# Kernel tuning notes

Hardware: AMD Instinct MI355X
Metric: run time of the kernel (lower is better)

Reference implementation:

```python
import jax, jax.numpy as jnp
import numpy as np

S, B, I, H, L = 256, 64, 512, 512, 2
EPS = 1e-5


def _layer_norm(x, g, b):
    m = jnp.mean(x, axis=-1, keepdims=True)
    v = jnp.var(x, axis=-1, keepdims=True)
    return (x - m) * jax.lax.rsqrt(v + EPS) * g + b


def setup_inputs() -> dict:
    key = jax.random.key(0)
    ks = jax.random.split(key, 8)
    gain = float(np.sqrt(1.0 / H))
    inputs = jax.random.normal(ks[0], (S, B, I), dtype=jnp.float32)
    h0 = jnp.zeros((L, B, H), dtype=jnp.float32)
    c0 = jnp.zeros((L, B, H), dtype=jnp.float32)
    # stacked weights (input_size == hidden_size so wx is uniform across layers)
    wx = jax.random.uniform(ks[1], (L, I, 4 * H), minval=-gain, maxval=gain, dtype=jnp.float32)
    wh = jax.random.uniform(ks[2], (L, H, 4 * H), minval=-gain, maxval=gain, dtype=jnp.float32)
    bias = jax.random.uniform(ks[3], (L, 4 * H), minval=-gain, maxval=gain, dtype=jnp.float32)
    # LayerNorm affine params: norm[2l] applied to x@wx, norm[2l+1] applied to h@wh
    ln_gx = jnp.ones((L, 4 * H), dtype=jnp.float32)
    ln_bx = jnp.zeros((L, 4 * H), dtype=jnp.float32)
    ln_gh = jnp.ones((L, 4 * H), dtype=jnp.float32)
    ln_bh = jnp.zeros((L, 4 * H), dtype=jnp.float32)
    return {"inputs": inputs, "h0": h0, "c0": c0, "wx": wx, "wh": wh,
            "bias": bias, "ln_gx": ln_gx, "ln_bx": ln_bx, "ln_gh": ln_gh, "ln_bh": ln_bh}


def reference(inputs, h0, c0, wx, wh, bias, ln_gx, ln_bx, ln_gh, ln_bh):
    x = inputs  # [S, B, I]
    hs, cs = [], []
    for l in range(L):
        # input-to-gate projection + its LayerNorm is time-independent: precompute
        xw = jnp.einsum('sbi,io->sbo', x, wx[l])            # [S, B, 4H]
        xn = _layer_norm(xw, ln_gx[l], ln_bx[l]) + bias[l]  # [S, B, 4H]
        whl, gh, bh = wh[l], ln_gh[l], ln_bh[l]

        def step(carry, xt):
            h, c = carry
            gate = xt + _layer_norm(h @ whl, gh, bh)        # [B, 4H]
            i, f, o, u = jnp.split(gate, 4, axis=-1)
            c = jax.nn.sigmoid(f) * c + jax.nn.sigmoid(i) * jnp.tanh(u)
            h = jax.nn.sigmoid(o) * jnp.tanh(c)
            return (h, c), h

        (hN, cN), ys = jax.lax.scan(step, (h0[l], c0[l]), xn)
        hs.append(hN)
        cs.append(cN)
        x = ys  # [S, B, H]
    h_n = jnp.stack(hs, axis=0)  # [L, B, H]
    c_n = jnp.stack(cs, axis=0)
    return x, h_n, c_n
```

## Files before the change

### kernel.cpp

```cpp
#include <hip/hip_runtime.h>

typedef unsigned short u16;
typedef _Float16 f16;
typedef __attribute__((ext_vector_type(8))) _Float16 f16x8;
typedef __attribute__((ext_vector_type(8))) unsigned short u16x8;
typedef __attribute__((ext_vector_type(4))) float f32x4;
typedef __attribute__((ext_vector_type(4))) unsigned u32x4;

#define NWG 32

__device__ __forceinline__ unsigned split2(float v) {
  f16 h = (f16)v;
  f16 l2 = (f16)((v - (float)h) * 2048.0f);
  return (unsigned)__builtin_bit_cast(u16, h) | ((unsigned)__builtin_bit_cast(u16, l2) << 16);
}

__global__ void k_zero(unsigned long long* __restrict__ ist, unsigned* __restrict__ flg) {
  int i = blockIdx.x * blockDim.x + threadIdx.x;
  if (i < 256) ist[i] = 0ull;
  if (i < 8192) flg[i] = 0u;
}

__global__ void k_wsplit(const float* __restrict__ wx, u16* __restrict__ th, u16* __restrict__ tl) {
  __shared__ float tile[32][33];
  int l = blockIdx.z;
  int n0 = blockIdx.x * 32, k0 = blockIdx.y * 32;
  int tx = threadIdx.x, ty = threadIdx.y;
  const float* src = wx + (size_t)l * 512 * 2048;
#pragma unroll
  for (int i = 0; i < 4; ++i)
    tile[ty + i * 8][tx] = src[(size_t)(k0 + ty + i * 8) * 2048 + n0 + tx];
  __syncthreads();
  u16* dh = th + (size_t)l * 2048 * 512;
  u16* dl = tl + (size_t)l * 2048 * 512;
#pragma unroll
  for (int i = 0; i < 4; ++i) {
    unsigned s = split2(tile[tx][ty + i * 8]);
    dh[(size_t)(n0 + ty + i * 8) * 512 + k0 + tx] = (u16)s;
    dl[(size_t)(n0 + ty + i * 8) * 512 + k0 + tx] = (u16)(s >> 16);
  }
}

__global__ void k_wlo(const float* __restrict__ wh, u16* __restrict__ wlo) {
  int idx = blockIdx.x * blockDim.x + threadIdx.x;
  int l = idx >> 17;
  int r = idx & 131071;
  int lane = r & 63;
  int fg = r >> 6;
  int kc = fg & 15, q = (fg >> 4) & 3, g = fg >> 6;
  int gcol = g * 16 + (lane & 15) + q * 512;
  int kb = kc * 32 + ((lane >> 4) << 3);
  const float* W = wh + (size_t)l * 512 * 2048;
  u16x8 o;
#pragma unroll
  for (int j = 0; j < 8; ++j)
    o[j] = (u16)(split2(W[(size_t)(kb + j) * 2048 + gcol]) >> 16);
  *(u16x8*)(wlo + (size_t)idx * 8) = o;
}

__global__ void __launch_bounds__(256, 1) k_gemm3(const float* __restrict__ A,
                                                  const u16* __restrict__ Bh, const u16* __restrict__ Bl,
                                                  float* __restrict__ C, int N, int K) {
  __shared__ u16 sA[2][128 * 64];
  __shared__ u16 sB[2][128 * 64];
  const int tid = threadIdx.x, l = tid & 63, w = tid >> 6;
  const int bx = blockIdx.x, by = blockIdx.y;
  const int wr = (w >> 1) * 64, wc = (w & 1) * 64;
  f32x4 acc0[4][4] = {}, acc1[4][4] = {};
  for (int k0 = 0; k0 < K; k0 += 64) {
#pragma unroll
    for (int s = 0; s < 4; ++s) {
      int cn = s * 256 + tid;
      int row = cn >> 3;
      int f0 = (cn & 7) * 8;
      int kb = f0 * 2;
      int sw = row * 128 + (kb ^ ((row & 7) << 4));
      const float* ap = A + ((size_t)(by * 128 + row) * K + k0 + f0);
      float4 a0 = *(const float4*)ap, a1 = *(const float4*)(ap + 4);
      float av[8] = {a0.x, a0.y, a0.z, a0.w, a1.x, a1.y, a1.z, a1.w};
      u16x8 ah_, al_;
#pragma unroll
      for (int j = 0; j < 8; ++j) {
        unsigned sp = split2(av[j]);
        ah_[j] = (u16)sp;
        al_[j] = (u16)(sp >> 16);
      }
      *(u16x8*)((char*)sA[0] + sw) = ah_;
      *(u16x8*)((char*)sA[1] + sw) = al_;
      size_t gb = (((size_t)(bx * 128 + row) * K + k0) << 1) + kb;
      *(u16x8*)((char*)sB[0] + sw) = *(const u16x8*)((const char*)Bh + gb);
      *(u16x8*)((char*)sB[1] + sw) = *(const u16x8*)((const char*)Bl + gb);
    }
    __syncthreads();
#pragma unroll
    for (int kc = 0; kc < 2; ++kc) {
      int kb = kc * 64 + (l >> 4) * 16;
      f16x8 ah[4], al[4], bh[4], bl[4];
#pragma unroll
      for (int mt = 0; mt < 4; ++mt) {
        int row = wr + mt * 16 + (l & 15);
        int off = row * 128 + (kb ^ ((row & 7) << 4));
        ah[mt] = *(const f16x8*)((const char*)sA[0] + off);
        al[mt] = *(const f16x8*)((const char*)sA[1] + off);
      }
#pragma unroll
      for (int nt = 0; nt < 4; ++nt) {
        int col = wc + nt * 16 + (l & 15);
        int off = col * 128 + (kb ^ ((col & 7) << 4));
        bh[nt] = *(const f16x8*)((const char*)sB[0] + off);
        bl[nt] = *(const f16x8*)((const char*)sB[1] + off);
      }
#pragma unroll
      for (int mt = 0; mt < 4; ++mt)
#pragma unroll
        for (int nt = 0; nt < 4; ++nt) {
          acc0[mt][nt] = __builtin_amdgcn_mfma_f32_16x16x32_f16(ah[mt], bh[nt], acc0[mt][nt], 0, 0, 0);
          acc1[mt][nt] = __builtin_amdgcn_mfma_f32_16x16x32_f16(ah[mt], bl[nt], acc1[mt][nt], 0, 0, 0);
          acc1[mt][nt] = __builtin_amdgcn_mfma_f32_16x16x32_f16(al[mt], bh[nt], acc1[mt][nt], 0, 0, 0);
        }
    }
    __syncthreads();
  }
#pragma unroll
  for (int mt = 0; mt < 4; ++mt)
#pragma unroll
    for (int nt = 0; nt < 4; ++nt)
#pragma unroll
      for (int j = 0; j < 4; ++j) {
        int row = by * 128 + wr + mt * 16 + ((l >> 4) << 2) + j;
        int col = bx * 128 + wc + nt * 16 + (l & 15);
        C[(size_t)row * N + col] = acc0[mt][nt][j] + acc1[mt][nt][j] * (1.0f / 2048.0f);
      }
}

__global__ void __launch_bounds__(256) k_ln2(float* __restrict__ X, const float* __restrict__ g,
                                             const float* __restrict__ b, const float* __restrict__ bias) {
  const int row = blockIdx.x, tid = threadIdx.x;
  float* rp = X + (size_t)row * 2048 + tid * 8;
  float4 v0 = *(const float4*)rp, v1 = *(const float4*)(rp + 4);
  float x[8] = {v0.x, v0.y, v0.z, v0.w, v1.x, v1.y, v1.z, v1.w};
  float s1 = 0.f, s2 = 0.f;
#pragma unroll
  for (int j = 0; j < 8; ++j) { s1 += x[j]; s2 += x[j] * x[j]; }
#pragma unroll
  for (int m = 1; m <= 32; m <<= 1) { s1 += __shfl_xor(s1, m, 64); s2 += __shfl_xor(s2, m, 64); }
  __shared__ float a1[4], a2[4];
  if ((tid & 63) == 0) { a1[tid >> 6] = s1; a2[tid >> 6] = s2; }
  __syncthreads();
  s1 = a1[0] + a1[1] + a1[2] + a1[3];
  s2 = a2[0] + a2[1] + a2[2] + a2[3];
  float mu = s1 * (1.f / 2048.f);
  float var = s2 * (1.f / 2048.f) - mu * mu;
  float rstd = 1.0f / sqrtf(var + 1e-5f);
#pragma unroll
  for (int j = 0; j < 8; ++j) {
    int c = tid * 8 + j;
    x[j] = (x[j] - mu) * rstd * g[c] + b[c] + bias[c];
  }
  *(float4*)rp = {x[0], x[1], x[2], x[3]};
  *(float4*)(rp + 4) = {x[4], x[5], x[6], x[7]};
}

__global__ void __launch_bounds__(256, 1) k_scan4(
    const float* __restrict__ wh, const u16* __restrict__ wlo,
    const float* __restrict__ gh, const float* __restrict__ bh,
    const float* __restrict__ xn, const float* __restrict__ h0l, const float* __restrict__ c0l,
    unsigned* __restrict__ hpubp, float* __restrict__ cspill,
    unsigned long long* __restrict__ istats, unsigned* __restrict__ flags,
    float* __restrict__ ys, float* __restrict__ hn, float* __restrict__ cn,
    int t0, int first) {
  __shared__ u16 pk[32768];
  __shared__ float musd[128];
  const int tid = threadIdx.x;
  const int l = tid & 63, w = tid >> 6;
  const int g = blockIdx.x;
  const int lq = l >> 4, ll = l & 15;
  const int hcol = g * 16 + ll;

  for (int c = tid; c < 4096; c += 256) {
    int lane = c & 63, kc = (c >> 6) & 15, q = c >> 10;
    int gcol = g * 16 + (lane & 15) + q * 512;
    int kb = kc * 32 + ((lane >> 4) << 3);
    u16x8 t8;
#pragma unroll
    for (int j = 0; j < 8; ++j)
      t8[j] = __builtin_bit_cast(u16, (f16)wh[(size_t)(kb + j) * 2048 + gcol]);
    *(u16x8*)(pk + (size_t)c * 8) = t8;
  }
  const u16* wloG = wlo + (size_t)g * 32768;
  float gam[4], bet[4];
#pragma unroll
  for (int q = 0; q < 4; ++q) { int gc = hcol + q * 512; gam[q] = gh[gc]; bet[q] = bh[gc]; }
  float cr[4];
#pragma unroll
  for (int j = 0; j < 4; ++j) {
    int r = w * 16 + lq * 4 + j;
    cr[j] = first ? c0l[r * 512 + hcol] : cspill[r * 512 + hcol];
  }
  if (first) {
    for (int u = tid; u < 1024; u += 256) {
      int row = 2 * g + (u >> 9), col = u & 511;
      __hip_atomic_store(&hpubp[row * 512 + col], split2(h0l[row * 512 + col]),
                         __ATOMIC_RELAXED, __HIP_MEMORY_SCOPE_AGENT);
    }
  }
  unsigned bid = 0;
#define BAR_ARRIVE()                                                                         \
  do {                                                                                       \
    bid++;                                                                                   \
    asm volatile("s_waitcnt vmcnt(0)" ::: "memory");                                         \
    __syncthreads();                                                                         \
    if (tid == 0)                                                                            \
      __hip_atomic_store(&flags[g * 32], bid, __ATOMIC_RELAXED, __HIP_MEMORY_SCOPE_AGENT);   \
  } while (0)
#define BAR_WAIT()                                                                           \
  do {                                                                                       \
    if (tid < NWG)                                                                           \
      while (__hip_atomic_load(&flags[tid * 32], __ATOMIC_RELAXED,                           \
                               __HIP_MEMORY_SCOPE_AGENT) < bid) {}                           \
    __builtin_amdgcn_fence(__ATOMIC_ACQUIRE, "agent");                                       \
  } while (0)

  BAR_ARRIVE();
  BAR_WAIT();
  __syncthreads();

  for (int t = 0; t < 128; ++t) {
    const int p = (t0 + t) & 1;
    f32x4 acc0[4] = {}, acc1[4] = {};
#pragma unroll
    for (int kc = 0; kc < 16; ++kc) {
      const unsigned* hp = hpubp + ((size_t)(w * 16 + ll) * 512 + kc * 32 + lq * 8);
      uint4 pa = *(const uint4*)hp;
      uint4 pb = *(const uint4*)(hp + 4);
      u32x4 ahw, alw;
      ahw[0] = __builtin_amdgcn_perm(pa.y, pa.x, 0x05040100u);
      ahw[1] = __builtin_amdgcn_perm(pa.w, pa.z, 0x05040100u);
      ahw[2] = __builtin_amdgcn_perm(pb.y, pb.x, 0x05040100u);
      ahw[3] = __builtin_amdgcn_perm(pb.w, pb.z, 0x05040100u);
      alw[0] = __builtin_amdgcn_perm(pa.y, pa.x, 0x07060302u);
      alw[1] = __builtin_amdgcn_perm(pa.w, pa.z, 0x07060302u);
      alw[2] = __builtin_amdgcn_perm(pb.y, pb.x, 0x07060302u);
      alw[3] = __builtin_amdgcn_perm(pb.w, pb.z, 0x07060302u);
      f16x8 ah = __builtin_bit_cast(f16x8, ahw);
      f16x8 al = __builtin_bit_cast(f16x8, alw);
#pragma unroll
      for (int q = 0; q < 4; ++q) {
        f16x8 bhv = *(const f16x8*)(pk + ((size_t)(q * 16 + kc) * 64 + l) * 8);
        f16x8 blv = *(const f16x8*)(wloG + ((size_t)(q * 16 + kc) * 64 + l) * 8);
        acc0[q] = __builtin_amdgcn_mfma_f32_16x16x32_f16(ah, bhv, acc0[q], 0, 0, 0);
        acc1[q] = __builtin_amdgcn_mfma_f32_16x16x32_f16(ah, blv, acc1[q], 0, 0, 0);
        acc1[q] = __builtin_amdgcn_mfma_f32_16x16x32_f16(al, bhv, acc1[q], 0, 0, 0);
      }
    }
    float y[4][4];
#pragma unroll
    for (int q = 0; q < 4; ++q)
#pragma unroll
      for (int j = 0; j < 4; ++j)
        y[q][j] = acc0[q][j] + acc1[q][j] * (1.0f / 2048.0f);

    float s1[4], s2[4];
#pragma unroll
    for (int j = 0; j < 4; ++j) {
      s1[j] = y[0][j] + y[1][j] + y[2][j] + y[3][j];
      s2[j] = y[0][j] * y[0][j] + y[1][j] * y[1][j] + y[2][j] * y[2][j] + y[3][j] * y[3][j];
    }
#pragma unroll
    for (int m = 1; m <= 8; m <<= 1)
#pragma unroll
      for (int j = 0; j < 4; ++j) {
        s1[j] += __shfl_xor(s1[j], m, 64);
        s2[j] += __shfl_xor(s2[j], m, 64);
      }
    if (ll < 8) {
      int j = ll >> 1;
      int r = w * 16 + lq * 4 + j;
      float v = (ll & 1) ? s2[j] : s1[j];
      long long qv = (long long)((double)v * 4294967296.0);
      atomicAdd(&istats[p * 128 + r * 2 + (ll & 1)], (unsigned long long)qv);
    }
    BAR_ARRIVE();
    float xp[16];
    {
      const float* xrow = xn + (size_t)t * 64 * 2048;
#pragma unroll
      for (int q = 0; q < 4; ++q)
#pragma unroll
        for (int j = 0; j < 4; ++j)
          xp[q * 4 + j] = xrow[(size_t)(w * 16 + lq * 4 + j) * 2048 + hcol + q * 512];
    }
    BAR_WAIT();
    if (tid < 64) {
      long long a1 = (long long)__hip_atomic_load(&istats[p * 128 + tid * 2], __ATOMIC_RELAXED,
                                                  __HIP_MEMORY_SCOPE_AGENT);
      long long a2 = (long long)__hip_atomic_load(&istats[p * 128 + tid * 2 + 1], __ATOMIC_RELAXED,
                                                  __HIP_MEMORY_SCOPE_AGENT);
      float mu = (float)((double)a1 * (1.0 / (4294967296.0 * 2048.0)));
      float ex2 = (float)((double)a2 * (1.0 / (4294967296.0 * 2048.0)));
      musd[tid] = mu;
      musd[64 + tid] = 1.0f / sqrtf(ex2 - mu * mu + 1e-5f);
    }
    __syncthreads();
    if (tid < 4)
      __hip_atomic_store(&istats[(1 - p) * 128 + g * 4 + tid], 0ull, __ATOMIC_RELAXED,
                         __HIP_MEMORY_SCOPE_AGENT);
#pragma unroll
    for (int j = 0; j < 4; ++j) {
      int r = w * 16 + lq * 4 + j;
      float mu = musd[r], rstd = musd[64 + r];
      float gv[4];
#pragma unroll
      for (int q = 0; q < 4; ++q)
        gv[q] = (y[q][j] - mu) * rstd * gam[q] + bet[q] + xp[q * 4 + j];
      float fi = 1.f / (1.f + expf(-gv[0]));
      float ff = 1.f / (1.f + expf(-gv[1]));
      float fo = 1.f / (1.f + expf(-gv[2]));
      float fu = tanhf(gv[3]);
      cr[j] = ff * cr[j] + fi * fu;
      float h = fo * tanhf(cr[j]);
      unsigned s = split2(h);
      size_t ro = (size_t)r * 512 + hcol;
      __hip_atomic_store(&hpubp[ro], s, __ATOMIC_RELAXED, __HIP_MEMORY_SCOPE_AGENT);
      __hip_atomic_store(&ys[(size_t)t * 32768 + ro], h, __ATOMIC_RELAXED, __HIP_MEMORY_SCOPE_AGENT);
      if (t == 127)
        __hip_atomic_store(&cspill[ro], cr[j], __ATOMIC_RELAXED, __HIP_MEMORY_SCOPE_AGENT);
      if (t0 + t == 255) {
        __hip_atomic_store(&hn[ro], h, __ATOMIC_RELAXED, __HIP_MEMORY_SCOPE_AGENT);
        __hip_atomic_store(&cn[ro], cr[j], __ATOMIC_RELAXED, __HIP_MEMORY_SCOPE_AGENT);
      }
    }
    BAR_ARRIVE();
    BAR_WAIT();
    __syncthreads();
  }
#undef BAR_ARRIVE
#undef BAR_WAIT
}

#define XN_OFF  0ull
#define WXH_OFF 67108864ull
#define WXL_OFF 71303168ull
#define WLO_OFF 75497472ull
#define HPP_OFF 79691776ull
#define CSP_OFF 79822848ull
#define IST_OFF 79953920ull
#define FLG_OFF 79955968ull

extern "C" void kernel_launch(void* const* d_in, const int* in_sizes, int n_in,
                              void* d_out, int out_size, void* d_ws, size_t ws_size,
                              hipStream_t stream) {
  const float* inputs = (const float*)d_in[0];
  const float* h0 = (const float*)d_in[1];
  const float* c0 = (const float*)d_in[2];
  const float* wx = (const float*)d_in[3];
  const float* wh = (const float*)d_in[4];
  const float* bias = (const float*)d_in[5];
  const float* gx = (const float*)d_in[6];
  const float* bxp = (const float*)d_in[7];
  const float* ghp = (const float*)d_in[8];
  const float* bhp = (const float*)d_in[9];
  float* out = (float*)d_out;
  char* ws = (char*)d_ws;

  float* xn = (float*)(ws + XN_OFF);
  u16* wxh = (u16*)(ws + WXH_OFF);
  u16* wxl = (u16*)(ws + WXL_OFF);
  u16* wlo = (u16*)(ws + WLO_OFF);
  unsigned* hpp = (unsigned*)(ws + HPP_OFF);
  float* csp = (float*)(ws + CSP_OFF);
  unsigned long long* ist = (unsigned long long*)(ws + IST_OFF);
  unsigned* flg = (unsigned*)(ws + FLG_OFF);

  k_zero<<<32, 256, 0, stream>>>(ist, flg);
  k_wsplit<<<dim3(64, 16, 2), dim3(32, 8), 0, stream>>>(wx, wxh, wxl);
  k_wlo<<<1024, 256, 0, stream>>>(wh, wlo);

  for (int l = 0; l < 2; ++l) {
    const float* Abase = (l == 0) ? inputs : out;
    for (int k = 0; k < 2; ++k) {
      k_gemm3<<<dim3(16, 64), 256, 0, stream>>>(Abase + (size_t)k * 8192 * 512,
                                                wxh + (size_t)l * 2048 * 512,
                                                wxl + (size_t)l * 2048 * 512, xn, 2048, 512);
      k_ln2<<<8192, 256, 0, stream>>>(xn, gx + l * 2048, bxp + l * 2048, bias + l * 2048);
      k_scan4<<<NWG, 256, 0, stream>>>(wh + (size_t)l * 1048576, wlo + (size_t)l * 1048576,
                                       ghp + l * 2048, bhp + l * 2048, xn,
                                       h0 + (size_t)l * 32768, c0 + (size_t)l * 32768,
                                       hpp, csp, ist, flg + (size_t)(l * 2 + k) * 2048,
                                       out + (size_t)k * 128 * 32768,
                                       out + 8388608 + (size_t)l * 32768,
                                       out + 8388608 + 65536 + (size_t)l * 32768,
                                       k * 128, (k == 0) ? 1 : 0);
    }
  }
}
```

Baseline: 7.427 ms.

## Replace atomic LayerNorm stat reduction with per-workgroup partials and prefetch next xn

```diff
diff --git a/kernel.cpp b/kernel.cpp
--- a/kernel.cpp
+++ b/kernel.cpp
@@ -15,10 +15,9 @@
   return (unsigned)__builtin_bit_cast(u16, h) | ((unsigned)__builtin_bit_cast(u16, l2) << 16);
 }
 
-__global__ void k_zero(unsigned long long* __restrict__ ist, unsigned* __restrict__ flg) {
+__global__ void k_zero(unsigned* __restrict__ part, unsigned* __restrict__ flg) {
   int i = blockIdx.x * blockDim.x + threadIdx.x;
-  if (i < 256) ist[i] = 0ull;
-  if (i < 8192) flg[i] = 0u;
+  if (i < 8192) { part[i] = 0u; flg[i] = 0u; }
 }
 
 __global__ void k_wsplit(const float* __restrict__ wx, u16* __restrict__ th, u16* __restrict__ tl) {
@@ -161,12 +160,12 @@
   *(float4*)(rp + 4) = {x[4], x[5], x[6], x[7]};
 }
 
-__global__ void __launch_bounds__(256, 1) k_scan4(
+__global__ void __launch_bounds__(256, 1) k_scan5(
     const float* __restrict__ wh, const u16* __restrict__ wlo,
     const float* __restrict__ gh, const float* __restrict__ bh,
     const float* __restrict__ xn, const float* __restrict__ h0l, const float* __restrict__ c0l,
     unsigned* __restrict__ hpubp, float* __restrict__ cspill,
-    unsigned long long* __restrict__ istats, unsigned* __restrict__ flags,
+    unsigned long long* __restrict__ part, unsigned* __restrict__ flags,
     float* __restrict__ ys, float* __restrict__ hn, float* __restrict__ cn,
     int t0, int first) {
   __shared__ u16 pk[32768];
@@ -221,7 +220,13 @@
     __builtin_amdgcn_fence(__ATOMIC_ACQUIRE, "agent");                                       \
   } while (0)
 
+  float xp[16];
   BAR_ARRIVE();
+#pragma unroll
+  for (int q = 0; q < 4; ++q)
+#pragma unroll
+    for (int j = 0; j < 4; ++j)
+      xp[q * 4 + j] = xn[(size_t)(w * 16 + lq * 4 + j) * 2048 + hcol + q * 512];
   BAR_WAIT();
   __syncthreads();
 
@@ -273,38 +278,33 @@
         s1[j] += __shfl_xor(s1[j], m, 64);
         s2[j] += __shfl_xor(s2[j], m, 64);
       }
-    if (ll < 8) {
-      int j = ll >> 1;
-      int r = w * 16 + lq * 4 + j;
-      float v = (ll & 1) ? s2[j] : s1[j];
-      long long qv = (long long)((double)v * 4294967296.0);
-      atomicAdd(&istats[p * 128 + r * 2 + (ll & 1)], (unsigned long long)qv);
+    if (ll == 0) {
+      unsigned long long* pp = part + ((size_t)p * 32 + g) * 64 + (w * 16 + lq * 4);
+#pragma unroll
+      for (int j = 0; j < 4; ++j) {
+        unsigned long long pv = ((unsigned long long)__builtin_bit_cast(unsigned, s2[j]) << 32) |
+                                (unsigned long long)__builtin_bit_cast(unsigned, s1[j]);
+        __hip_atomic_store(&pp[j], pv, __ATOMIC_RELAXED, __HIP_MEMORY_SCOPE_AGENT);
+      }
     }
     BAR_ARRIVE();
-    float xp[16];
-    {
-      const float* xrow = xn + (size_t)t * 64 * 2048;
-#pragma unroll
-      for (int q = 0; q < 4; ++q)
-#pragma unroll
-        for (int j = 0; j < 4; ++j)
-          xp[q * 4 + j] = xrow[(size_t)(w * 16 + lq * 4 + j) * 2048 + hcol + q * 512];
-    }
     BAR_WAIT();
     if (tid < 64) {
-      long long a1 = (long long)__hip_atomic_load(&istats[p * 128 + tid * 2], __ATOMIC_RELAXED,
-                                                  __HIP_MEMORY_SCOPE_AGENT);
-      long long a2 = (long long)__hip_atomic_load(&istats[p * 128 + tid * 2 + 1], __ATOMIC_RELAXED,
-                                                  __HIP_MEMORY_SCOPE_AGENT);
-      float mu = (float)((double)a1 * (1.0 / (4294967296.0 * 2048.0)));
-      float ex2 = (float)((double)a2 * (1.0 / (4294967296.0 * 2048.0)));
+      float a1 = 0.f, a2 = 0.f;
+      const unsigned long long* pp = part + (size_t)p * 2048 + tid;
+#pragma unroll 8
+      for (int gg = 0; gg < 32; ++gg) {
+        unsigned long long v = pp[(size_t)gg * 64];
+        a1 += __builtin_bit_cast(float, (unsigned)v);
+        a2 += __builtin_bit_cast(float, (unsigned)(v >> 32));
+      }
+      float mu = a1 * (1.f / 2048.f);
+      float ex2 = a2 * (1.f / 2048.f);
       musd[tid] = mu;
       musd[64 + tid] = 1.0f / sqrtf(ex2 - mu * mu + 1e-5f);
     }
     __syncthreads();
-    if (tid < 4)
-      __hip_atomic_store(&istats[(1 - p) * 128 + g * 4 + tid], 0ull, __ATOMIC_RELAXED,
-                         __HIP_MEMORY_SCOPE_AGENT);
+    float hs[4];
 #pragma unroll
     for (int j = 0; j < 4; ++j) {
       int r = w * 16 + lq * 4 + j;
@@ -319,18 +319,31 @@
       float fu = tanhf(gv[3]);
       cr[j] = ff * cr[j] + fi * fu;
       float h = fo * tanhf(cr[j]);
-      unsigned s = split2(h);
+      hs[j] = h;
+      __hip_atomic_store(&hpubp[(size_t)r * 512 + hcol], split2(h),
+                         __ATOMIC_RELAXED, __HIP_MEMORY_SCOPE_AGENT);
+    }
+    BAR_ARRIVE();
+#pragma unroll
+    for (int j = 0; j < 4; ++j) {
+      int r = w * 16 + lq * 4 + j;
       size_t ro = (size_t)r * 512 + hcol;
-      __hip_atomic_store(&hpubp[ro], s, __ATOMIC_RELAXED, __HIP_MEMORY_SCOPE_AGENT);
-      __hip_atomic_store(&ys[(size_t)t * 32768 + ro], h, __ATOMIC_RELAXED, __HIP_MEMORY_SCOPE_AGENT);
+      __hip_atomic_store(&ys[(size_t)t * 32768 + ro], hs[j], __ATOMIC_RELAXED, __HIP_MEMORY_SCOPE_AGENT);
       if (t == 127)
         __hip_atomic_store(&cspill[ro], cr[j], __ATOMIC_RELAXED, __HIP_MEMORY_SCOPE_AGENT);
       if (t0 + t == 255) {
-        __hip_atomic_store(&hn[ro], h, __ATOMIC_RELAXED, __HIP_MEMORY_SCOPE_AGENT);
+        __hip_atomic_store(&hn[ro], hs[j], __ATOMIC_RELAXED, __HIP_MEMORY_SCOPE_AGENT);
         __hip_atomic_store(&cn[ro], cr[j], __ATOMIC_RELAXED, __HIP_MEMORY_SCOPE_AGENT);
       }
     }
-    BAR_ARRIVE();
+    if (t < 127) {
+      const float* xrow = xn + (size_t)(t + 1) * 64 * 2048;
+#pragma unroll
+      for (int q = 0; q < 4; ++q)
+#pragma unroll
+        for (int j = 0; j < 4; ++j)
+          xp[q * 4 + j] = xrow[(size_t)(w * 16 + lq * 4 + j) * 2048 + hcol + q * 512];
+    }
     BAR_WAIT();
     __syncthreads();
   }
@@ -338,14 +351,14 @@
 #undef BAR_WAIT
 }
 
-#define XN_OFF  0ull
-#define WXH_OFF 67108864ull
-#define WXL_OFF 71303168ull
-#define WLO_OFF 75497472ull
-#define HPP_OFF 79691776ull
-#define CSP_OFF 79822848ull
-#define IST_OFF 79953920ull
-#define FLG_OFF 79955968ull
+#define XN_OFF   0ull
+#define WXH_OFF  67108864ull
+#define WXL_OFF  71303168ull
+#define WLO_OFF  75497472ull
+#define HPP_OFF  79691776ull
+#define CSP_OFF  79822848ull
+#define PART_OFF 79953920ull
+#define FLG_OFF  79986688ull
 
 extern "C" void kernel_launch(void* const* d_in, const int* in_sizes, int n_in,
                               void* d_out, int out_size, void* d_ws, size_t ws_size,
@@ -369,10 +382,10 @@
   u16* wlo = (u16*)(ws + WLO_OFF);
   unsigned* hpp = (unsigned*)(ws + HPP_OFF);
   float* csp = (float*)(ws + CSP_OFF);
-  unsigned long long* ist = (unsigned long long*)(ws + IST_OFF);
+  unsigned long long* part = (unsigned long long*)(ws + PART_OFF);
   unsigned* flg = (unsigned*)(ws + FLG_OFF);
 
-  k_zero<<<32, 256, 0, stream>>>(ist, flg);
+  k_zero<<<32, 256, 0, stream>>>((unsigned*)(ws + PART_OFF), flg);
   k_wsplit<<<dim3(64, 16, 2), dim3(32, 8), 0, stream>>>(wx, wxh, wxl);
   k_wlo<<<1024, 256, 0, stream>>>(wh, wlo);
 
@@ -383,10 +396,10 @@
                                                 wxh + (size_t)l * 2048 * 512,
                                                 wxl + (size_t)l * 2048 * 512, xn, 2048, 512);
       k_ln2<<<8192, 256, 0, stream>>>(xn, gx + l * 2048, bxp + l * 2048, bias + l * 2048);
-      k_scan4<<<NWG, 256, 0, stream>>>(wh + (size_t)l * 1048576, wlo + (size_t)l * 1048576,
+      k_scan5<<<NWG, 256, 0, stream>>>(wh + (size_t)l * 1048576, wlo + (size_t)l * 1048576,
                                        ghp + l * 2048, bhp + l * 2048, xn,
                                        h0 + (size_t)l * 32768, c0 + (size_t)l * 32768,
-                                       hpp, csp, ist, flg + (size_t)(l * 2 + k) * 2048,
+                                       hpp, csp, part, flg + (size_t)(l * 2 + k) * 2048,
                                        out + (size_t)k * 128 * 32768,
                                        out + 8388608 + (size_t)l * 32768,
                                        out + 8388608 + 65536 + (size_t)l * 32768,
```

Result: slower. 11.18 ms (+50.6%).

## Fuse both LSTM layers and input projection into one wavefront-pipelined persistent scan

Applied to the files above, without the earlier changes.

```diff
diff --git a/kernel.cpp b/kernel.cpp
--- a/kernel.cpp
+++ b/kernel.cpp
@@ -7,7 +7,7 @@
 typedef __attribute__((ext_vector_type(4))) float f32x4;
 typedef __attribute__((ext_vector_type(4))) unsigned u32x4;
 
-#define NWG 32
+#define NWGT 64
 
 __device__ __forceinline__ unsigned split2(float v) {
   f16 h = (f16)v;
@@ -15,194 +15,89 @@
   return (unsigned)__builtin_bit_cast(u16, h) | ((unsigned)__builtin_bit_cast(u16, l2) << 16);
 }
 
-__global__ void k_zero(unsigned long long* __restrict__ ist, unsigned* __restrict__ flg) {
+__global__ void k_zero(unsigned* __restrict__ flg) {
   int i = blockIdx.x * blockDim.x + threadIdx.x;
-  if (i < 256) ist[i] = 0ull;
-  if (i < 8192) flg[i] = 0u;
-}
-
-__global__ void k_wsplit(const float* __restrict__ wx, u16* __restrict__ th, u16* __restrict__ tl) {
-  __shared__ float tile[32][33];
-  int l = blockIdx.z;
-  int n0 = blockIdx.x * 32, k0 = blockIdx.y * 32;
-  int tx = threadIdx.x, ty = threadIdx.y;
-  const float* src = wx + (size_t)l * 512 * 2048;
-#pragma unroll
-  for (int i = 0; i < 4; ++i)
-    tile[ty + i * 8][tx] = src[(size_t)(k0 + ty + i * 8) * 2048 + n0 + tx];
-  __syncthreads();
-  u16* dh = th + (size_t)l * 2048 * 512;
-  u16* dl = tl + (size_t)l * 2048 * 512;
-#pragma unroll
-  for (int i = 0; i < 4; ++i) {
-    unsigned s = split2(tile[tx][ty + i * 8]);
-    dh[(size_t)(n0 + ty + i * 8) * 512 + k0 + tx] = (u16)s;
-    dl[(size_t)(n0 + ty + i * 8) * 512 + k0 + tx] = (u16)(s >> 16);
-  }
-}
-
-__global__ void k_wlo(const float* __restrict__ wh, u16* __restrict__ wlo) {
+  if (i < 2048) flg[i] = 0u;
+}
+
+__global__ void k_xsplit(const float* __restrict__ in, unsigned* __restrict__ out, int n) {
+  for (int i = blockIdx.x * blockDim.x + threadIdx.x; i < n; i += gridDim.x * blockDim.x)
+    out[i] = split2(in[i]);
+}
+
+__global__ void k_pack(const float* __restrict__ W, u16* __restrict__ hi, u16* __restrict__ lo) {
   int idx = blockIdx.x * blockDim.x + threadIdx.x;
-  int l = idx >> 17;
-  int r = idx & 131071;
-  int lane = r & 63;
-  int fg = r >> 6;
-  int kc = fg & 15, q = (fg >> 4) & 3, g = fg >> 6;
+  int lane = idx & 63, kc = (idx >> 6) & 15, q = (idx >> 10) & 3, g = idx >> 12;
   int gcol = g * 16 + (lane & 15) + q * 512;
   int kb = kc * 32 + ((lane >> 4) << 3);
-  const float* W = wh + (size_t)l * 512 * 2048;
-  u16x8 o;
-#pragma unroll
-  for (int j = 0; j < 8; ++j)
-    o[j] = (u16)(split2(W[(size_t)(kb + j) * 2048 + gcol]) >> 16);
-  *(u16x8*)(wlo + (size_t)idx * 8) = o;
-}
-
-__global__ void __launch_bounds__(256, 1) k_gemm3(const float* __restrict__ A,
-                                                  const u16* __restrict__ Bh, const u16* __restrict__ Bl,
-                                                  float* __restrict__ C, int N, int K) {
-  __shared__ u16 sA[2][128 * 64];
-  __shared__ u16 sB[2][128 * 64];
-  const int tid = threadIdx.x, l = tid & 63, w = tid >> 6;
-  const int bx = blockIdx.x, by = blockIdx.y;
-  const int wr = (w >> 1) * 64, wc = (w & 1) * 64;
-  f32x4 acc0[4][4] = {}, acc1[4][4] = {};
-  for (int k0 = 0; k0 < K; k0 += 64) {
-#pragma unroll
-    for (int s = 0; s < 4; ++s) {
-      int cn = s * 256 + tid;
-      int row = cn >> 3;
-      int f0 = (cn & 7) * 8;
-      int kb = f0 * 2;
-      int sw = row * 128 + (kb ^ ((row & 7) << 4));
-      const float* ap = A + ((size_t)(by * 128 + row) * K + k0 + f0);
-      float4 a0 = *(const float4*)ap, a1 = *(const float4*)(ap + 4);
-      float av[8] = {a0.x, a0.y, a0.z, a0.w, a1.x, a1.y, a1.z, a1.w};
-      u16x8 ah_, al_;
-#pragma unroll
-      for (int j = 0; j < 8; ++j) {
-        unsigned sp = split2(av[j]);
-        ah_[j] = (u16)sp;
-        al_[j] = (u16)(sp >> 16);
-      }
-      *(u16x8*)((char*)sA[0] + sw) = ah_;
-      *(u16x8*)((char*)sA[1] + sw) = al_;
-      size_t gb = (((size_t)(bx * 128 + row) * K + k0) << 1) + kb;
-      *(u16x8*)((char*)sB[0] + sw) = *(const u16x8*)((const char*)Bh + gb);
-      *(u16x8*)((char*)sB[1] + sw) = *(const u16x8*)((const char*)Bl + gb);
-    }
-    __syncthreads();
-#pragma unroll
-    for (int kc = 0; kc < 2; ++kc) {
-      int kb = kc * 64 + (l >> 4) * 16;
-      f16x8 ah[4], al[4], bh[4], bl[4];
-#pragma unroll
-      for (int mt = 0; mt < 4; ++mt) {
-        int row = wr + mt * 16 + (l & 15);
-        int off = row * 128 + (kb ^ ((row & 7) << 4));
-        ah[mt] = *(const f16x8*)((const char*)sA[0] + off);
-        al[mt] = *(const f16x8*)((const char*)sA[1] + off);
-      }
-#pragma unroll
-      for (int nt = 0; nt < 4; ++nt) {
-        int col = wc + nt * 16 + (l & 15);
-        int off = col * 128 + (kb ^ ((col & 7) << 4));
-        bh[nt] = *(const f16x8*)((const char*)sB[0] + off);
-        bl[nt] = *(const f16x8*)((const char*)sB[1] + off);
-      }
-#pragma unroll
-      for (int mt = 0; mt < 4; ++mt)
-#pragma unroll
-        for (int nt = 0; nt < 4; ++nt) {
-          acc0[mt][nt] = __builtin_amdgcn_mfma_f32_16x16x32_f16(ah[mt], bh[nt], acc0[mt][nt], 0, 0, 0);
-          acc1[mt][nt] = __builtin_amdgcn_mfma_f32_16x16x32_f16(ah[mt], bl[nt], acc1[mt][nt], 0, 0, 0);
-          acc1[mt][nt] = __builtin_amdgcn_mfma_f32_16x16x32_f16(al[mt], bh[nt], acc1[mt][nt], 0, 0, 0);
-        }
-    }
-    __syncthreads();
-  }
-#pragma unroll
-  for (int mt = 0; mt < 4; ++mt)
-#pragma unroll
-    for (int nt = 0; nt < 4; ++nt)
-#pragma unroll
-      for (int j = 0; j < 4; ++j) {
-        int row = by * 128 + wr + mt * 16 + ((l >> 4) << 2) + j;
-        int col = bx * 128 + wc + nt * 16 + (l & 15);
-        C[(size_t)row * N + col] = acc0[mt][nt][j] + acc1[mt][nt][j] * (1.0f / 2048.0f);
-      }
-}
-
-__global__ void __launch_bounds__(256) k_ln2(float* __restrict__ X, const float* __restrict__ g,
-                                             const float* __restrict__ b, const float* __restrict__ bias) {
-  const int row = blockIdx.x, tid = threadIdx.x;
-  float* rp = X + (size_t)row * 2048 + tid * 8;
-  float4 v0 = *(const float4*)rp, v1 = *(const float4*)(rp + 4);
-  float x[8] = {v0.x, v0.y, v0.z, v0.w, v1.x, v1.y, v1.z, v1.w};
-  float s1 = 0.f, s2 = 0.f;
-#pragma unroll
-  for (int j = 0; j < 8; ++j) { s1 += x[j]; s2 += x[j] * x[j]; }
-#pragma unroll
-  for (int m = 1; m <= 32; m <<= 1) { s1 += __shfl_xor(s1, m, 64); s2 += __shfl_xor(s2, m, 64); }
-  __shared__ float a1[4], a2[4];
-  if ((tid & 63) == 0) { a1[tid >> 6] = s1; a2[tid >> 6] = s2; }
-  __syncthreads();
-  s1 = a1[0] + a1[1] + a1[2] + a1[3];
-  s2 = a2[0] + a2[1] + a2[2] + a2[3];
-  float mu = s1 * (1.f / 2048.f);
-  float var = s2 * (1.f / 2048.f) - mu * mu;
-  float rstd = 1.0f / sqrtf(var + 1e-5f);
+  u16x8 oh, ol;
 #pragma unroll
   for (int j = 0; j < 8; ++j) {
-    int c = tid * 8 + j;
-    x[j] = (x[j] - mu) * rstd * g[c] + b[c] + bias[c];
-  }
-  *(float4*)rp = {x[0], x[1], x[2], x[3]};
-  *(float4*)(rp + 4) = {x[4], x[5], x[6], x[7]};
-}
-
-__global__ void __launch_bounds__(256, 1) k_scan4(
-    const float* __restrict__ wh, const u16* __restrict__ wlo,
+    unsigned s = split2(W[(size_t)(kb + j) * 2048 + gcol]);
+    oh[j] = (u16)s;
+    ol[j] = (u16)(s >> 16);
+  }
+  *(u16x8*)(hi + (size_t)idx * 8) = oh;
+  *(u16x8*)(lo + (size_t)idx * 8) = ol;
+}
+
+__device__ __forceinline__ void unpk(uint4 a, uint4 b, f16x8& hi, f16x8& lo) {
+  u32x4 H, L;
+  H[0] = __builtin_amdgcn_perm(a.y, a.x, 0x05040100u);
+  H[1] = __builtin_amdgcn_perm(a.w, a.z, 0x05040100u);
+  H[2] = __builtin_amdgcn_perm(b.y, b.x, 0x05040100u);
+  H[3] = __builtin_amdgcn_perm(b.w, b.z, 0x05040100u);
+  L[0] = __builtin_amdgcn_perm(a.y, a.x, 0x07060302u);
+  L[1] = __builtin_amdgcn_perm(a.w, a.z, 0x07060302u);
+  L[2] = __builtin_amdgcn_perm(b.y, b.x, 0x07060302u);
+  L[3] = __builtin_amdgcn_perm(b.w, b.z, 0x07060302u);
+  hi = __builtin_bit_cast(f16x8, H);
+  lo = __builtin_bit_cast(f16x8, L);
+}
+
+__global__ void __launch_bounds__(256, 1) k_scan7(
+    const unsigned* __restrict__ xs, const u16* __restrict__ frg,
+    const float* __restrict__ gx, const float* __restrict__ bx,
     const float* __restrict__ gh, const float* __restrict__ bh,
-    const float* __restrict__ xn, const float* __restrict__ h0l, const float* __restrict__ c0l,
-    unsigned* __restrict__ hpubp, float* __restrict__ cspill,
-    unsigned long long* __restrict__ istats, unsigned* __restrict__ flags,
-    float* __restrict__ ys, float* __restrict__ hn, float* __restrict__ cn,
-    int t0, int first) {
-  __shared__ u16 pk[32768];
-  __shared__ float musd[128];
+    const float* __restrict__ bias,
+    const float* __restrict__ h0, const float* __restrict__ c0,
+    unsigned* __restrict__ hpub0, unsigned* __restrict__ hpub1,
+    unsigned long long* __restrict__ part, unsigned* __restrict__ flags,
+    float* __restrict__ out) {
+  __shared__ u16 pkh[32768];
+  __shared__ u16 pkx[32768];
+  __shared__ float musd[256];
   const int tid = threadIdx.x;
   const int l = tid & 63, w = tid >> 6;
   const int g = blockIdx.x;
+  const int layer = g >> 5, gg = g & 31;
   const int lq = l >> 4, ll = l & 15;
-  const int hcol = g * 16 + ll;
-
+  const int hcol = gg * 16 + ll;
+  const bool l0 = (layer == 0);
+
+  const u16* whh_g = frg + (size_t)(layer * 4 + 0) * 1048576 + (size_t)gg * 32768;
+  const u16* whl_g = frg + (size_t)(layer * 4 + 1) * 1048576 + (size_t)gg * 32768;
+  const u16* wxh_g = frg + (size_t)(layer * 4 + 2) * 1048576 + (size_t)gg * 32768;
+  const u16* wxl_g = frg + (size_t)(layer * 4 + 3) * 1048576 + (size_t)gg * 32768;
   for (int c = tid; c < 4096; c += 256) {
-    int lane = c & 63, kc = (c >> 6) & 15, q = c >> 10;
-    int gcol = g * 16 + (lane & 15) + q * 512;
-    int kb = kc * 32 + ((lane >> 4) << 3);
-    u16x8 t8;
-#pragma unroll
-    for (int j = 0; j < 8; ++j)
-      t8[j] = __builtin_bit_cast(u16, (f16)wh[(size_t)(kb + j) * 2048 + gcol]);
-    *(u16x8*)(pk + (size_t)c * 8) = t8;
-  }
-  const u16* wloG = wlo + (size_t)g * 32768;
-  float gam[4], bet[4];
-#pragma unroll
-  for (int q = 0; q < 4; ++q) { int gc = hcol + q * 512; gam[q] = gh[gc]; bet[q] = bh[gc]; }
+    *(u16x8*)(pkh + (size_t)c * 8) = *(const u16x8*)(whh_g + (size_t)c * 8);
+    *(u16x8*)(pkx + (size_t)c * 8) = *(const u16x8*)(wxh_g + (size_t)c * 8);
+  }
+  float gxv[4], bxv[4], ghv[4], bhv[4], biv[4];
+#pragma unroll
+  for (int q = 0; q < 4; ++q) {
+    int gc = layer * 2048 + hcol + q * 512;
+    gxv[q] = gx[gc]; bxv[q] = bx[gc]; ghv[q] = gh[gc]; bhv[q] = bh[gc]; biv[q] = bias[gc];
+  }
   float cr[4];
 #pragma unroll
-  for (int j = 0; j < 4; ++j) {
-    int r = w * 16 + lq * 4 + j;
-    cr[j] = first ? c0l[r * 512 + hcol] : cspill[r * 512 + hcol];
-  }
-  if (first) {
-    for (int u = tid; u < 1024; u += 256) {
-      int row = 2 * g + (u >> 9), col = u & 511;
-      __hip_atomic_store(&hpubp[row * 512 + col], split2(h0l[row * 512 + col]),
-                         __ATOMIC_RELAXED, __HIP_MEMORY_SCOPE_AGENT);
-    }
+  for (int j = 0; j < 4; ++j)
+    cr[j] = c0[layer * 32768 + (w * 16 + lq * 4 + j) * 512 + hcol];
+  unsigned* myhp = l0 ? hpub0 : hpub1;
+  for (int u = tid; u < 1024; u += 256) {
+    int row = 2 * gg + (u >> 9), col = u & 511;
+    __hip_atomic_store(&myhp[row * 512 + col], split2(h0[layer * 32768 + row * 512 + col]),
+                       __ATOMIC_RELAXED, __HIP_MEMORY_SCOPE_AGENT);
   }
   unsigned bid = 0;
 #define BAR_ARRIVE()                                                                         \
@@ -215,7 +110,7 @@
   } while (0)
 #define BAR_WAIT()                                                                           \
   do {                                                                                       \
-    if (tid < NWG)                                                                           \
+    if (tid < NWGT)                                                                          \
       while (__hip_atomic_load(&flags[tid * 32], __ATOMIC_RELAXED,                           \
                                __HIP_MEMORY_SCOPE_AGENT) < bid) {}                           \
     __builtin_amdgcn_fence(__ATOMIC_ACQUIRE, "agent");                                       \
@@ -225,127 +120,147 @@
   BAR_WAIT();
   __syncthreads();
 
-  for (int t = 0; t < 128; ++t) {
-    const int p = (t0 + t) & 1;
-    f32x4 acc0[4] = {}, acc1[4] = {};
-#pragma unroll
-    for (int kc = 0; kc < 16; ++kc) {
-      const unsigned* hp = hpubp + ((size_t)(w * 16 + ll) * 512 + kc * 32 + lq * 8);
-      uint4 pa = *(const uint4*)hp;
-      uint4 pb = *(const uint4*)(hp + 4);
-      u32x4 ahw, alw;
-      ahw[0] = __builtin_amdgcn_perm(pa.y, pa.x, 0x05040100u);
-      ahw[1] = __builtin_amdgcn_perm(pa.w, pa.z, 0x05040100u);
-      ahw[2] = __builtin_amdgcn_perm(pb.y, pb.x, 0x05040100u);
-      ahw[3] = __builtin_amdgcn_perm(pb.w, pb.z, 0x05040100u);
-      alw[0] = __builtin_amdgcn_perm(pa.y, pa.x, 0x07060302u);
-      alw[1] = __builtin_amdgcn_perm(pa.w, pa.z, 0x07060302u);
-      alw[2] = __builtin_amdgcn_perm(pb.y, pb.x, 0x07060302u);
-      alw[3] = __builtin_amdgcn_perm(pb.w, pb.z, 0x07060302u);
-      f16x8 ah = __builtin_bit_cast(f16x8, ahw);
-      f16x8 al = __builtin_bit_cast(f16x8, alw);
-#pragma unroll
-      for (int q = 0; q < 4; ++q) {
-        f16x8 bhv = *(const f16x8*)(pk + ((size_t)(q * 16 + kc) * 64 + l) * 8);
-        f16x8 blv = *(const f16x8*)(wloG + ((size_t)(q * 16 + kc) * 64 + l) * 8);
-        acc0[q] = __builtin_amdgcn_mfma_f32_16x16x32_f16(ah, bhv, acc0[q], 0, 0, 0);
-        acc1[q] = __builtin_amdgcn_mfma_f32_16x16x32_f16(ah, blv, acc1[q], 0, 0, 0);
-        acc1[q] = __builtin_amdgcn_mfma_f32_16x16x32_f16(al, bhv, acc1[q], 0, 0, 0);
-      }
-    }
-    float y[4][4];
-#pragma unroll
-    for (int q = 0; q < 4; ++q)
-#pragma unroll
-      for (int j = 0; j < 4; ++j)
-        y[q][j] = acc0[q][j] + acc1[q][j] * (1.0f / 2048.0f);
-
-    float s1[4], s2[4];
-#pragma unroll
-    for (int j = 0; j < 4; ++j) {
-      s1[j] = y[0][j] + y[1][j] + y[2][j] + y[3][j];
-      s2[j] = y[0][j] * y[0][j] + y[1][j] * y[1][j] + y[2][j] * y[2][j] + y[3][j] * y[3][j];
-    }
-#pragma unroll
-    for (int m = 1; m <= 8; m <<= 1)
+  for (int s = 0; s < 257; ++s) {
+    const int t = l0 ? s : s - 1;
+    const bool act = l0 ? (s < 256) : (s >= 1);
+    const int p = s & 1;
+    float yx[4][4], yh[4][4];
+    if (act) {
+      const unsigned* xbase = l0 ? (xs + (size_t)t * 32768) : hpub0;
+      const unsigned* hbase = l0 ? hpub0 : hpub1;
+      f32x4 ax0[4] = {}, ax1[4] = {}, ah0[4] = {}, ah1[4] = {};
+#pragma unroll
+      for (int kc = 0; kc < 16; ++kc) {
+        size_t aoff = (size_t)(w * 16 + ll) * 512 + kc * 32 + lq * 8;
+        uint4 xa = *(const uint4*)(xbase + aoff), xb = *(const uint4*)(xbase + aoff + 4);
+        uint4 ha = *(const uint4*)(hbase + aoff), hb = *(const uint4*)(hbase + aoff + 4);
+        f16x8 xah, xal, hah, hal;
+        unpk(xa, xb, xah, xal);
+        unpk(ha, hb, hah, hal);
+#pragma unroll
+        for (int q = 0; q < 4; ++q) {
+          size_t fo = ((size_t)(q * 16 + kc) * 64 + l) * 8;
+          f16x8 wxhf = *(const f16x8*)(pkx + fo);
+          f16x8 wxlf = *(const f16x8*)(wxl_g + fo);
+          f16x8 whhf = *(const f16x8*)(pkh + fo);
+          f16x8 whlf = *(const f16x8*)(whl_g + fo);
+          ax0[q] = __builtin_amdgcn_mfma_f32_16x16x32_f16(xah, wxhf, ax0[q], 0, 0, 0);
+          ax1[q] = __builtin_amdgcn_mfma_f32_16x16x32_f16(xah, wxlf, ax1[q], 0, 0, 0);
+          ax1[q] = __builtin_amdgcn_mfma_f32_16x16x32_f16(xal, wxhf, ax1[q], 0, 0, 0);
+          ah0[q] = __builtin_amdgcn_mfma_f32_16x16x32_f16(hah, whhf, ah0[q], 0, 0, 0);
+          ah1[q] = __builtin_amdgcn_mfma_f32_16x16x32_f16(hah, whlf, ah1[q], 0, 0, 0);
+          ah1[q] = __builtin_amdgcn_mfma_f32_16x16x32_f16(hal, whhf, ah1[q], 0, 0, 0);
+        }
+      }
+#pragma unroll
+      for (int q = 0; q < 4; ++q)
+#pragma unroll
+        for (int j = 0; j < 4; ++j) {
+          yx[q][j] = ax0[q][j] + ax1[q][j] * (1.0f / 2048.0f);
+          yh[q][j] = ah0[q][j] + ah1[q][j] * (1.0f / 2048.0f);
+        }
+      float s1x[4], s2x[4], s1h[4], s2h[4];
 #pragma unroll
       for (int j = 0; j < 4; ++j) {
-        s1[j] += __shfl_xor(s1[j], m, 64);
-        s2[j] += __shfl_xor(s2[j], m, 64);
-      }
-    if (ll < 8) {
-      int j = ll >> 1;
-      int r = w * 16 + lq * 4 + j;
-      float v = (ll & 1) ? s2[j] : s1[j];
-      long long qv = (long long)((double)v * 4294967296.0);
-      atomicAdd(&istats[p * 128 + r * 2 + (ll & 1)], (unsigned long long)qv);
-    }
-    BAR_ARRIVE();
-    float xp[16];
-    {
-      const float* xrow = xn + (size_t)t * 64 * 2048;
-#pragma unroll
-      for (int q = 0; q < 4; ++q)
-#pragma unroll
-        for (int j = 0; j < 4; ++j)
-          xp[q * 4 + j] = xrow[(size_t)(w * 16 + lq * 4 + j) * 2048 + hcol + q * 512];
-    }
-    BAR_WAIT();
-    if (tid < 64) {
-      long long a1 = (long long)__hip_atomic_load(&istats[p * 128 + tid * 2], __ATOMIC_RELAXED,
-                                                  __HIP_MEMORY_SCOPE_AGENT);
-      long long a2 = (long long)__hip_atomic_load(&istats[p * 128 + tid * 2 + 1], __ATOMIC_RELAXED,
-                                                  __HIP_MEMORY_SCOPE_AGENT);
-      float mu = (float)((double)a1 * (1.0 / (4294967296.0 * 2048.0)));
-      float ex2 = (float)((double)a2 * (1.0 / (4294967296.0 * 2048.0)));
-      musd[tid] = mu;
-      musd[64 + tid] = 1.0f / sqrtf(ex2 - mu * mu + 1e-5f);
-    }
-    __syncthreads();
-    if (tid < 4)
-      __hip_atomic_store(&istats[(1 - p) * 128 + g * 4 + tid], 0ull, __ATOMIC_RELAXED,
-                         __HIP_MEMORY_SCOPE_AGENT);
-#pragma unroll
-    for (int j = 0; j < 4; ++j) {
-      int r = w * 16 + lq * 4 + j;
-      float mu = musd[r], rstd = musd[64 + r];
-      float gv[4];
-#pragma unroll
-      for (int q = 0; q < 4; ++q)
-        gv[q] = (y[q][j] - mu) * rstd * gam[q] + bet[q] + xp[q * 4 + j];
-      float fi = 1.f / (1.f + expf(-gv[0]));
-      float ff = 1.f / (1.f + expf(-gv[1]));
-      float fo = 1.f / (1.f + expf(-gv[2]));
-      float fu = tanhf(gv[3]);
-      cr[j] = ff * cr[j] + fi * fu;
-      float h = fo * tanhf(cr[j]);
-      unsigned s = split2(h);
-      size_t ro = (size_t)r * 512 + hcol;
-      __hip_atomic_store(&hpubp[ro], s, __ATOMIC_RELAXED, __HIP_MEMORY_SCOPE_AGENT);
-      __hip_atomic_store(&ys[(size_t)t * 32768 + ro], h, __ATOMIC_RELAXED, __HIP_MEMORY_SCOPE_AGENT);
-      if (t == 127)
-        __hip_atomic_store(&cspill[ro], cr[j], __ATOMIC_RELAXED, __HIP_MEMORY_SCOPE_AGENT);
-      if (t0 + t == 255) {
-        __hip_atomic_store(&hn[ro], h, __ATOMIC_RELAXED, __HIP_MEMORY_SCOPE_AGENT);
-        __hip_atomic_store(&cn[ro], cr[j], __ATOMIC_RELAXED, __HIP_MEMORY_SCOPE_AGENT);
+        s1x[j] = yx[0][j] + yx[1][j] + yx[2][j] + yx[3][j];
+        s2x[j] = yx[0][j] * yx[0][j] + yx[1][j] * yx[1][j] + yx[2][j] * yx[2][j] + yx[3][j] * yx[3][j];
+        s1h[j] = yh[0][j] + yh[1][j] + yh[2][j] + yh[3][j];
+        s2h[j] = yh[0][j] * yh[0][j] + yh[1][j] * yh[1][j] + yh[2][j] * yh[2][j] + yh[3][j] * yh[3][j];
+      }
+#pragma unroll
+      for (int m = 1; m <= 8; m <<= 1)
+#pragma unroll
+        for (int j = 0; j < 4; ++j) {
+          s1x[j] += __shfl_xor(s1x[j], m, 64);
+          s2x[j] += __shfl_xor(s2x[j], m, 64);
+          s1h[j] += __shfl_xor(s1h[j], m, 64);
+          s2h[j] += __shfl_xor(s2h[j], m, 64);
+        }
+      if (ll == 0) {
+#pragma unroll
+        for (int j = 0; j < 4; ++j) {
+          int r = w * 16 + lq * 4 + j;
+          size_t bx_ = ((((size_t)layer * 2 + p) * 2 + 0) * 64 + r) * 32 + gg;
+          size_t bh_ = ((((size_t)layer * 2 + p) * 2 + 1) * 64 + r) * 32 + gg;
+          unsigned long long vx = ((unsigned long long)__builtin_bit_cast(unsigned, s2x[j]) << 32) |
+                                  (unsigned long long)__builtin_bit_cast(unsigned, s1x[j]);
+          unsigned long long vh = ((unsigned long long)__builtin_bit_cast(unsigned, s2h[j]) << 32) |
+                                  (unsigned long long)__builtin_bit_cast(unsigned, s1h[j]);
+          __hip_atomic_store(&part[bx_], vx, __ATOMIC_RELAXED, __HIP_MEMORY_SCOPE_AGENT);
+          __hip_atomic_store(&part[bh_], vh, __ATOMIC_RELAXED, __HIP_MEMORY_SCOPE_AGENT);
+        }
       }
     }
     BAR_ARRIVE();
     BAR_WAIT();
+    float hs[4];
+    if (act) {
+      if (tid < 64) {
+        const uint4* px = (const uint4*)(part + ((((size_t)layer * 2 + p) * 2 + 0) * 64 + tid) * 32);
+        const uint4* ph = (const uint4*)(part + ((((size_t)layer * 2 + p) * 2 + 1) * 64 + tid) * 32);
+        float a1x = 0.f, a2x = 0.f, a1h = 0.f, a2h = 0.f;
+#pragma unroll
+        for (int i = 0; i < 16; ++i) {
+          uint4 vx = px[i], vh = ph[i];
+          a1x += __builtin_bit_cast(float, vx.x); a2x += __builtin_bit_cast(float, vx.y);
+          a1x += __builtin_bit_cast(float, vx.z); a2x += __builtin_bit_cast(float, vx.w);
+          a1h += __builtin_bit_cast(float, vh.x); a2h += __builtin_bit_cast(float, vh.y);
+          a1h += __builtin_bit_cast(float, vh.z); a2h += __builtin_bit_cast(float, vh.w);
+        }
+        float mux = a1x * (1.f / 2048.f), ex2x = a2x * (1.f / 2048.f);
+        float muh = a1h * (1.f / 2048.f), ex2h = a2h * (1.f / 2048.f);
+        musd[tid] = mux;
+        musd[64 + tid] = 1.0f / sqrtf(ex2x - mux * mux + 1e-5f);
+        musd[128 + tid] = muh;
+        musd[192 + tid] = 1.0f / sqrtf(ex2h - muh * muh + 1e-5f);
+      }
+      __syncthreads();
+#pragma unroll
+      for (int j = 0; j < 4; ++j) {
+        int r = w * 16 + lq * 4 + j;
+        float mux = musd[r], rsx = musd[64 + r], muh = musd[128 + r], rsh = musd[192 + r];
+        float gv[4];
+#pragma unroll
+        for (int q = 0; q < 4; ++q)
+          gv[q] = (yx[q][j] - mux) * rsx * gxv[q] + bxv[q] + biv[q] +
+                  (yh[q][j] - muh) * rsh * ghv[q] + bhv[q];
+        float fi = 1.f / (1.f + expf(-gv[0]));
+        float ff = 1.f / (1.f + expf(-gv[1]));
+        float fo = 1.f / (1.f + expf(-gv[2]));
+        float fu = tanhf(gv[3]);
+        cr[j] = ff * cr[j] + fi * fu;
+        float h = fo * tanhf(cr[j]);
+        hs[j] = h;
+        __hip_atomic_store(&myhp[(size_t)r * 512 + hcol], split2(h),
+                           __ATOMIC_RELAXED, __HIP_MEMORY_SCOPE_AGENT);
+      }
+    }
+    BAR_ARRIVE();
+    if (act) {
+#pragma unroll
+      for (int j = 0; j < 4; ++j) {
+        int r = w * 16 + lq * 4 + j;
+        size_t ro = (size_t)r * 512 + hcol;
+        if (!l0) out[(size_t)t * 32768 + ro] = hs[j];
+        if (t == 255) {
+          out[8388608 + (size_t)layer * 32768 + ro] = hs[j];
+          out[8388608 + 65536 + (size_t)layer * 32768 + ro] = cr[j];
+        }
+      }
+    }
+    BAR_WAIT();
     __syncthreads();
   }
 #undef BAR_ARRIVE
 #undef BAR_WAIT
 }
 
-#define XN_OFF  0ull
-#define WXH_OFF 67108864ull
-#define WXL_OFF 71303168ull
-#define WLO_OFF 75497472ull
-#define HPP_OFF 79691776ull
-#define CSP_OFF 79822848ull
-#define IST_OFF 79953920ull
-#define FLG_OFF 79955968ull
+#define XS_OFF  0ull
+#define FRG_OFF 33554432ull
+#define HP0_OFF 50331648ull
+#define HP1_OFF 50462720ull
+#define PRT_OFF 50593792ull
+#define FLG_OFF 50855936ull
 
 extern "C" void kernel_launch(void* const* d_in, const int* in_sizes, int n_in,
                               void* d_out, int out_size, void* d_ws, size_t ws_size,
@@ -356,41 +271,30 @@
   const float* wx = (const float*)d_in[3];
   const float* wh = (const float*)d_in[4];
   const float* bias = (const float*)d_in[5];
-  const float* gx = (const float*)d_in[6];
+  const float* gxp = (const float*)d_in[6];
   const float* bxp = (const float*)d_in[7];
   const float* ghp = (const float*)d_in[8];
   const float* bhp = (const float*)d_in[9];
   float* out = (float*)d_out;
   char* ws = (char*)d_ws;
 
-  float* xn = (float*)(ws + XN_OFF);
-  u16* wxh = (u16*)(ws + WXH_OFF);
-  u16* wxl = (u16*)(ws + WXL_OFF);
-  u16* wlo = (u16*)(ws + WLO_OFF);
-  unsigned* hpp = (unsigned*)(ws + HPP_OFF);
-  float* csp = (float*)(ws + CSP_OFF);
-  unsigned long long* ist = (unsigned long long*)(ws + IST_OFF);
+  unsigned* xs = (unsigned*)(ws + XS_OFF);
+  u16* frg = (u16*)(ws + FRG_OFF);
+  unsigned* hp0 = (unsigned*)(ws + HP0_OFF);
+  unsigned* hp1 = (unsigned*)(ws + HP1_OFF);
+  unsigned long long* prt = (unsigned long long*)(ws + PRT_OFF);
   unsigned* flg = (unsigned*)(ws + FLG_OFF);
 
-  k_zero<<<32, 256, 0, stream>>>(ist, flg);
-  k_wsplit<<<dim3(64, 16, 2), dim3(32, 8), 0, stream>>>(wx, wxh, wxl);
-  k_wlo<<<1024, 256, 0, stream>>>(wh, wlo);
-
+  k_zero<<<8, 256, 0, stream>>>(flg);
+  k_xsplit<<<4096, 256, 0, stream>>>(inputs, xs, 8388608);
   for (int l = 0; l < 2; ++l) {
-    const float* Abase = (l == 0) ? inputs : out;
-    for (int k = 0; k < 2; ++k) {
-      k_gemm3<<<dim3(16, 64), 256, 0, stream>>>(Abase + (size_t)k * 8192 * 512,
-                                                wxh + (size_t)l * 2048 * 512,
-                                                wxl + (size_t)l * 2048 * 512, xn, 2048, 512);
-      k_ln2<<<8192, 256, 0, stream>>>(xn, gx + l * 2048, bxp + l * 2048, bias + l * 2048);
-      k_scan4<<<NWG, 256, 0, stream>>>(wh + (size_t)l * 1048576, wlo + (size_t)l * 1048576,
-                                       ghp + l * 2048, bhp + l * 2048, xn,
-                                       h0 + (size_t)l * 32768, c0 + (size_t)l * 32768,
-                                       hpp, csp, ist, flg + (size_t)(l * 2 + k) * 2048,
-                                       out + (size_t)k * 128 * 32768,
-                                       out + 8388608 + (size_t)l * 32768,
-                                       out + 8388608 + 65536 + (size_t)l * 32768,
-                                       k * 128, (k == 0) ? 1 : 0);
-    }
-  }
-}
+    k_pack<<<512, 256, 0, stream>>>(wh + (size_t)l * 1048576,
+                                    frg + (size_t)(l * 4 + 0) * 1048576,
+                                    frg + (size_t)(l * 4 + 1) * 1048576);
+    k_pack<<<512, 256, 0, stream>>>(wx + (size_t)l * 1048576,
+                                    frg + (size_t)(l * 4 + 2) * 1048576,
+                                    frg + (size_t)(l * 4 + 3) * 1048576);
+  }
+  k_scan7<<<NWGT, 256, 0, stream>>>(xs, frg, gxp, bxp, ghp, bhp, bias, h0, c0,
+                                    hp0, hp1, prt, flg, out);
+}
```

Result: slower. 8.831 ms, median of 5 (+18.9%).
